# Kernel optimization log

Hardware: AMD Instinct MI355X
Metric: run time of the kernel (lower is better)

Reference implementation:

```python
import jax, jax.numpy as jnp
import numpy as np

ALPHA = 0.2  # LeakyReLU negative slope


def setup_inputs() -> dict:
    key = jax.random.key(0)
    k1, k2, k3, k4 = jax.random.split(key, 4)
    N, IN, OUT = 8192, 512, 256
    x = jax.random.normal(k1, (N, IN), dtype=jnp.float32)
    adj = jnp.zeros((N, N), dtype=jnp.float32)  # accepted but unused by the module
    W = jax.random.normal(k2, (OUT, IN), dtype=jnp.float32) * (1.0 / np.sqrt(IN))
    a1 = jax.random.normal(k3, (OUT,), dtype=jnp.float32) * (1.0 / np.sqrt(OUT))
    a2 = jax.random.normal(k4, (OUT,), dtype=jnp.float32) * (1.0 / np.sqrt(OUT))
    return {"x": x, "adj": adj, "W": W, "a1": a1, "a2": a2}


def reference(x, adj, W, a1, a2):
    # h = tran(x): [N, OUT]
    h = x @ W.T
    # additive GAT scores: e[i, j] = a2 . h_i + a1 . h_j  (from unsqueeze(0)+unsqueeze(1))
    s1 = h @ a1  # [N], att1(h)
    s2 = h @ a2  # [N], att2(h)
    e = s2[:, None] + s1[None, :]  # [N, N]
    e = jnp.where(e > 0, e, ALPHA * e)  # LeakyReLU
    attn = jax.nn.softmax(e, axis=1)  # softmax over dim=1; dropout is identity in eval
    return attn @ h  # [N, OUT]
```

## Files before the change

kernel.cpp:

```cpp
#include <hip/hip_runtime.h>

#define NROW 8192
#define DIN  512
#define DOUT 256
#define NCHUNK 256
#define CLEN 32

constexpr size_t OFF_H      = 0;
constexpr size_t OFF_S1     = OFF_H + (size_t)NROW*DOUT*4;
constexpr size_t OFF_S2     = OFF_S1 + NROW*4;
constexpr size_t OFF_RANK   = OFF_S2 + NROW*4;
constexpr size_t OFF_MISC   = OFF_RANK + NROW*4;
constexpr size_t MEMSET_LEN = OFF_MISC + 256 - OFF_S1;
constexpr size_t OFF_S1S    = OFF_MISC + 256;
constexpr size_t OFF_PERM   = OFF_S1S + NROW*4;
constexpr size_t OFF_WHI    = OFF_PERM + NROW*4;
constexpr size_t OFF_WLO    = OFF_WHI + NROW*4;
constexpr size_t OFF_PRELOS = OFF_WLO + NROW*4;
constexpr size_t OFF_SUFHIS = OFF_PRELOS + 33024;
constexpr size_t OFF_CSLO   = OFF_SUFHIS + 33024;
constexpr size_t OFF_CSHI   = OFF_CSLO + 1024;
constexpr size_t OFF_TLO    = OFF_CSHI + 1024;
constexpr size_t OFF_THI    = OFF_TLO + (size_t)NCHUNK*DOUT*4;
constexpr size_t OFF_PRELO  = OFF_THI + (size_t)NCHUNK*DOUT*4;
constexpr size_t OFF_SUFHI  = OFF_PRELO + (size_t)(NROW+1)*DOUT*4;
constexpr size_t WS_NEED    = OFF_SUFHI + (size_t)(NROW+1)*DOUT*4;

__global__ __launch_bounds__(256) void gemm_h(const float* __restrict__ x,
                                              const float* __restrict__ W,
                                              const float* __restrict__ a1,
                                              const float* __restrict__ a2,
                                              float* __restrict__ h,
                                              float* __restrict__ s1,
                                              float* __restrict__ s2) {
  __shared__ float xs[64][68];
  __shared__ float ws[64][68];
  const int tid = threadIdx.x;
  const int rowBase = blockIdx.x * 64;
  const int colBase = blockIdx.y * 64;
  const int ty = tid >> 4, tx = tid & 15;
  float acc[4][4] = {};
  for (int k0 = 0; k0 < DIN; k0 += 64) {
#pragma unroll
    for (int i = 0; i < 4; ++i) {
      int s = i * 256 + tid;
      int r = s >> 4;
      int kk = (s & 15) << 2;
      float4 v = *(const float4*)(x + (size_t)(rowBase + r) * DIN + k0 + kk);
      xs[kk + 0][r] = v.x; xs[kk + 1][r] = v.y; xs[kk + 2][r] = v.z; xs[kk + 3][r] = v.w;
      float4 u = *(const float4*)(W + (size_t)(colBase + r) * DIN + k0 + kk);
      ws[kk + 0][r] = u.x; ws[kk + 1][r] = u.y; ws[kk + 2][r] = u.z; ws[kk + 3][r] = u.w;
    }
    __syncthreads();
#pragma unroll
    for (int kk = 0; kk < 64; ++kk) {
      float4 av = *(const float4*)&xs[kk][ty << 2];
      float4 bv = *(const float4*)&ws[kk][tx << 2];
      float a[4] = {av.x, av.y, av.z, av.w};
      float b[4] = {bv.x, bv.y, bv.z, bv.w};
#pragma unroll
      for (int r = 0; r < 4; ++r)
#pragma unroll
        for (int c = 0; c < 4; ++c) acc[r][c] = fmaf(a[r], b[c], acc[r][c]);
    }
    __syncthreads();
  }
#pragma unroll
  for (int r = 0; r < 4; ++r) {
    float4 o = make_float4(acc[r][0], acc[r][1], acc[r][2], acc[r][3]);
    *(float4*)(h + (size_t)(rowBase + (ty << 2) + r) * DOUT + colBase + (tx << 2)) = o;
  }
  float4 A1 = *(const float4*)(a1 + colBase + (tx << 2));
  float4 A2 = *(const float4*)(a2 + colBase + (tx << 2));
#pragma unroll
  for (int r = 0; r < 4; ++r) {
    float p1 = acc[r][0] * A1.x + acc[r][1] * A1.y + acc[r][2] * A1.z + acc[r][3] * A1.w;
    float p2 = acc[r][0] * A2.x + acc[r][1] * A2.y + acc[r][2] * A2.z + acc[r][3] * A2.w;
#pragma unroll
    for (int m = 1; m < 16; m <<= 1) {
      p1 += __shfl_xor(p1, m);
      p2 += __shfl_xor(p2, m);
    }
    if (tx == 0) {
      int row = rowBase + (ty << 2) + r;
      atomicAdd(&s1[row], p1);
      atomicAdd(&s2[row], p2);
    }
  }
}

__global__ __launch_bounds__(256) void rank_count(const float* __restrict__ s1,
                                                  int* __restrict__ rank,
                                                  unsigned int* __restrict__ miscu) {
  __shared__ float sj[1024];
  __shared__ float wm[4];
  const int t = threadIdx.x;
  const int ib = blockIdx.x, jc = blockIdx.y;
  const int j0 = jc * 1024;
  *(float4*)&sj[t << 2] = *(const float4*)(s1 + j0 + (t << 2));
  const int i = ib * 256 + t;
  const float v = s1[i];
  __syncthreads();
  int cnt = 0;
#pragma unroll 4
  for (int q = 0; q < 256; ++q) {
    float4 sv = *(const float4*)&sj[q << 2];
    int jg = j0 + (q << 2);
    cnt += (int)(sv.x < v) + (int)((sv.x == v) & (jg + 0 < i));
    cnt += (int)(sv.y < v) + (int)((sv.y == v) & (jg + 1 < i));
    cnt += (int)(sv.z < v) + (int)((sv.z == v) & (jg + 2 < i));
    cnt += (int)(sv.w < v) + (int)((sv.w == v) & (jg + 3 < i));
  }
  atomicAdd(&rank[i], cnt);
  if (jc == 0) {
    float m = v;
#pragma unroll
    for (int off = 32; off > 0; off >>= 1) m = fmaxf(m, __shfl_down(m, off));
    if ((t & 63) == 0) wm[t >> 6] = m;
    __syncthreads();
    if (t == 0) {
      float mm = fmaxf(fmaxf(wm[0], wm[1]), fmaxf(wm[2], wm[3]));
      unsigned int b = __float_as_uint(mm);
      unsigned int enc = (b & 0x80000000u) ? ~b : (b | 0x80000000u);
      atomicMax(miscu, enc);
    }
  }
}

__global__ __launch_bounds__(256) void scatter_w(const float* __restrict__ s1,
                                                 const int* __restrict__ rank,
                                                 const unsigned int* __restrict__ miscu,
                                                 float* __restrict__ miscf,
                                                 float* __restrict__ s1s,
                                                 int* __restrict__ perm,
                                                 float* __restrict__ w_hi,
                                                 float* __restrict__ w_lo) {
  const int i = blockIdx.x * 256 + threadIdx.x;
  unsigned int e = miscu[0];
  unsigned int b = (e & 0x80000000u) ? (e & 0x7fffffffu) : ~e;
  const float M1 = __uint_as_float(b);
  const float v = s1[i];
  const int r = rank[i];
  s1s[r] = v;
  perm[r] = i;
  w_hi[r] = __expf(v - M1);
  w_lo[r] = __expf(0.2f * (v - M1));
  if (i == 0) miscf[0] = M1;
}

__global__ __launch_bounds__(256) void chunk_totals(const float* __restrict__ h,
                                                    const int* __restrict__ perm,
                                                    const float* __restrict__ w_hi,
                                                    const float* __restrict__ w_lo,
                                                    float* __restrict__ T_lo,
                                                    float* __restrict__ T_hi,
                                                    float* __restrict__ cs_lo,
                                                    float* __restrict__ cs_hi) {
  const int d = threadIdx.x, b = blockIdx.x;
  const int j0 = b * CLEN;
  float tlo = 0.f, thi = 0.f;
#pragma unroll
  for (int e = 0; e < CLEN; e += 4) {
    int4 p4 = *(const int4*)(perm + j0 + e);
    float4 wl4 = *(const float4*)(w_lo + j0 + e);
    float4 wh4 = *(const float4*)(w_hi + j0 + e);
    float h0 = h[(size_t)p4.x * DOUT + d];
    float h1 = h[(size_t)p4.y * DOUT + d];
    float h2 = h[(size_t)p4.z * DOUT + d];
    float h3 = h[(size_t)p4.w * DOUT + d];
    tlo += wl4.x * h0 + wl4.y * h1 + wl4.z * h2 + wl4.w * h3;
    thi += wh4.x * h0 + wh4.y * h1 + wh4.z * h2 + wh4.w * h3;
  }
  T_lo[b * DOUT + d] = tlo;
  T_hi[b * DOUT + d] = thi;
  if (d < 64) {
    float wl = (d < 32) ? w_lo[j0 + d] : 0.f;
    float wh = (d < 32) ? w_hi[j0 + d] : 0.f;
#pragma unroll
    for (int off = 32; off > 0; off >>= 1) {
      wl += __shfl_down(wl, off);
      wh += __shfl_down(wh, off);
    }
    if (d == 0) { cs_lo[b] = wl; cs_hi[b] = wh; }
  }
}

__global__ __launch_bounds__(256) void write_prefix(const float* __restrict__ h,
                                                    const int* __restrict__ perm,
                                                    const float* __restrict__ w_hi,
                                                    const float* __restrict__ w_lo,
                                                    const float* __restrict__ T_lo,
                                                    const float* __restrict__ T_hi,
                                                    const float* __restrict__ cs_lo,
                                                    const float* __restrict__ cs_hi,
                                                    float* __restrict__ PreLo,
                                                    float* __restrict__ SufHi,
                                                    float* __restrict__ prelo_s,
                                                    float* __restrict__ sufhi_s) {
  const int d = threadIdx.x, b = blockIdx.x;
  const int j0 = b * CLEN;
  if (d < 64) {
    float accp = 0.f, acct = 0.f;
    for (int p = d; p < NCHUNK; p += 64) {
      float cl = cs_lo[p], ch = cs_hi[p];
      accp += (p < b) ? cl : 0.f;
      acct += (p > b) ? ch : 0.f;
    }
#pragma unroll
    for (int off = 32; off > 0; off >>= 1) {
      accp += __shfl_down(accp, off);
      acct += __shfl_down(acct, off);
    }
    float pres  = __shfl(accp, 0);
    float tails = __shfl(acct, 0);
    float wl = (d < 32) ? w_lo[j0 + d] : 0.f;
    float wh = (d < 32) ? w_hi[j0 + d] : 0.f;
    float pl = wl, ph = wh;
#pragma unroll
    for (int off = 1; off < 32; off <<= 1) {
      float a = __shfl_up(pl, off);
      float c = __shfl_up(ph, off);
      if (d >= off) { pl += a; ph += c; }
    }
    float chunk_hi_tot = __shfl(ph, 31);
    if (d < 32) {
      prelo_s[j0 + d] = pres + (pl - wl);
      sufhi_s[j0 + d] = tails + (chunk_hi_tot - (ph - wh));
    }
    if (b == NCHUNK - 1 && d == 31) {
      prelo_s[NROW] = pres + pl;
      sufhi_s[NROW] = 0.f;
    }
  }
  float rl = 0.f, tail = 0.f;
#pragma unroll 8
  for (int p = 0; p < NCHUNK; ++p) {
    float vl = T_lo[p * DOUT + d];
    float vh = T_hi[p * DOUT + d];
    rl   += (p < b) ? vl : 0.f;
    tail += (p > b) ? vh : 0.f;
  }
  float hv[CLEN], wlv[CLEN], whv[CLEN];
  float ownHi = 0.f;
#pragma unroll
  for (int e = 0; e < CLEN; e += 4) {
    int4 p4 = *(const int4*)(perm + j0 + e);
    float4 wl4 = *(const float4*)(w_lo + j0 + e);
    float4 wh4 = *(const float4*)(w_hi + j0 + e);
    hv[e + 0] = h[(size_t)p4.x * DOUT + d];
    hv[e + 1] = h[(size_t)p4.y * DOUT + d];
    hv[e + 2] = h[(size_t)p4.z * DOUT + d];
    hv[e + 3] = h[(size_t)p4.w * DOUT + d];
    wlv[e + 0] = wl4.x; wlv[e + 1] = wl4.y; wlv[e + 2] = wl4.z; wlv[e + 3] = wl4.w;
    whv[e + 0] = wh4.x; whv[e + 1] = wh4.y; whv[e + 2] = wh4.z; whv[e + 3] = wh4.w;
    ownHi += wh4.x * hv[e] + wh4.y * hv[e + 1] + wh4.z * hv[e + 2] + wh4.w * hv[e + 3];
  }
  float shb = tail + ownHi;
  float preh = 0.f;
#pragma unroll
  for (int e = 0; e < CLEN; ++e) {
    size_t j = (size_t)(j0 + e);
    PreLo[j * DOUT + d] = rl;
    SufHi[j * DOUT + d] = shb - preh;
    rl   += wlv[e] * hv[e];
    preh += whv[e] * hv[e];
  }
  if (b == NCHUNK - 1) {
    PreLo[(size_t)NROW * DOUT + d] = rl;
    SufHi[(size_t)NROW * DOUT + d] = 0.f;
  }
}

__global__ __launch_bounds__(256) void finalize(const float* __restrict__ s2,
                                                const float* __restrict__ s1s,
                                                const float* __restrict__ miscf,
                                                const float* __restrict__ PreLo,
                                                const float* __restrict__ SufHi,
                                                const float* __restrict__ prelo_s,
                                                const float* __restrict__ sufhi_s,
                                                float* __restrict__ out) {
  const int wave = threadIdx.x >> 6, lane = threadIdx.x & 63;
  const int i = blockIdx.x * 4 + wave;
  const float c = s2[i];
  const float M1 = miscf[0];
  const float tval = -c;
  int lo = 0, hi = NROW;
  while (lo < hi) {
    int mid = (lo + hi) >> 1;
    if (s1s[mid] <= tval) lo = mid + 1; else hi = mid;
  }
  const int k = lo;
  const float u = c + M1;
  const float m = fmaxf(u, 0.2f * u);
  const float fh = __expf(u - m);
  const float fl = __expf(0.2f * u - m);
  const float den = fh * sufhi_s[k] + fl * prelo_s[k];
  const float inv = 1.f / den;
  float4 A = *(const float4*)(SufHi + (size_t)k * DOUT + (lane << 2));
  float4 B = *(const float4*)(PreLo + (size_t)k * DOUT + (lane << 2));
  float4 o;
  o.x = (fh * A.x + fl * B.x) * inv;
  o.y = (fh * A.y + fl * B.y) * inv;
  o.z = (fh * A.z + fl * B.z) * inv;
  o.w = (fh * A.w + fl * B.w) * inv;
  *(float4*)(out + (size_t)i * DOUT + (lane << 2)) = o;
}

extern "C" void kernel_launch(void* const* d_in, const int* in_sizes, int n_in,
                              void* d_out, int out_size, void* d_ws, size_t ws_size,
                              hipStream_t stream) {
  const float* x  = (const float*)d_in[0];
  const float* W  = (const float*)d_in[2];
  const float* a1 = (const float*)d_in[3];
  const float* a2 = (const float*)d_in[4];
  float* out = (float*)d_out;

  char* ws = (char*)d_ws;
  if (ws_size < WS_NEED) ws = (char*)d_in[1];

  float*        h       = (float*)(ws + OFF_H);
  float*        s1      = (float*)(ws + OFF_S1);
  float*        s2      = (float*)(ws + OFF_S2);
  int*          rank    = (int*)  (ws + OFF_RANK);
  unsigned int* miscu   = (unsigned int*)(ws + OFF_MISC);
  float*        miscf   = (float*)(ws + OFF_MISC) + 1;
  float*        s1s     = (float*)(ws + OFF_S1S);
  int*          perm    = (int*)  (ws + OFF_PERM);
  float*        w_hi    = (float*)(ws + OFF_WHI);
  float*        w_lo    = (float*)(ws + OFF_WLO);
  float*        prelo_s = (float*)(ws + OFF_PRELOS);
  float*        sufhi_s = (float*)(ws + OFF_SUFHIS);
  float*        cs_lo   = (float*)(ws + OFF_CSLO);
  float*        cs_hi   = (float*)(ws + OFF_CSHI);
  float*        T_lo    = (float*)(ws + OFF_TLO);
  float*        T_hi    = (float*)(ws + OFF_THI);
  float*        PreLo   = (float*)(ws + OFF_PRELO);
  float*        SufHi   = (float*)(ws + OFF_SUFHI);

  hipMemsetAsync(s1, 0, MEMSET_LEN, stream);

  gemm_h<<<dim3(NROW / 64, DOUT / 64), 256, 0, stream>>>(x, W, a1, a2, h, s1, s2);
  rank_count<<<dim3(NROW / 256, 8), 256, 0, stream>>>(s1, rank, miscu);
  scatter_w<<<NROW / 256, 256, 0, stream>>>(s1, rank, miscu, miscf, s1s, perm, w_hi, w_lo);
  chunk_totals<<<NCHUNK, 256, 0, stream>>>(h, perm, w_hi, w_lo, T_lo, T_hi, cs_lo, cs_hi);
  write_prefix<<<NCHUNK, 256, 0, stream>>>(h, perm, w_hi, w_lo, T_lo, T_hi, cs_lo, cs_hi,
                                           PreLo, SufHi, prelo_s, sufhi_s);
  finalize<<<NROW / 4, 256, 0, stream>>>(s2, s1s, miscf, PreLo, SufHi, prelo_s, sufhi_s, out);
}
```

Measured before the change: 405.7 us.

## Replace FP32 GEMM with split-bf16 three-pass MFMA and separate score kernel

Rewrites the x·Wᵀ GEMM to use bf16 MFMA 16x16x32 instructions. It emulates FP32 accuracy with a three-pass hi/lo split (hi·hi, lo·hi, hi·lo), converting operands to bf16 in registers while staging them to shared memory. The attention-score dot products s1/s2 are moved out of the GEMM epilogue into a separate per-row kernel, which removes the atomics. This costs an extra kernel launch and an extra read of h, and the split-bf16 scheme drops the lo·lo term, so precision is slightly reduced.

```diff
diff --git a/kernel.cpp b/kernel.cpp
--- a/kernel.cpp
+++ b/kernel.cpp
@@ -26,67 +26,110 @@
 constexpr size_t OFF_SUFHI  = OFF_PRELO + (size_t)(NROW+1)*DOUT*4;
 constexpr size_t WS_NEED    = OFF_SUFHI + (size_t)(NROW+1)*DOUT*4;
 
-__global__ __launch_bounds__(256) void gemm_h(const float* __restrict__ x,
-                                              const float* __restrict__ W,
-                                              const float* __restrict__ a1,
-                                              const float* __restrict__ a2,
-                                              float* __restrict__ h,
-                                              float* __restrict__ s1,
-                                              float* __restrict__ s2) {
-  __shared__ float xs[64][68];
-  __shared__ float ws[64][68];
+typedef float f32x4 __attribute__((ext_vector_type(4)));
+typedef short s16x8 __attribute__((ext_vector_type(8)));
+
+__device__ __forceinline__ unsigned short bf16_rne(float f) {
+  unsigned int u = __float_as_uint(f);
+  return (unsigned short)((u + 0x7fffu + ((u >> 16) & 1u)) >> 16);
+}
+__device__ __forceinline__ unsigned short bf16_part(float f, bool lo) {
+  unsigned short hi = bf16_rne(f);
+  if (!lo) return hi;
+  float r = f - __uint_as_float(((unsigned int)hi) << 16);
+  return bf16_rne(r);
+}
+__device__ __forceinline__ s16x8 cvt8(const float4 u, const float4 v, bool lo) {
+  s16x8 r;
+  r[0] = (short)bf16_part(u.x, lo); r[1] = (short)bf16_part(u.y, lo);
+  r[2] = (short)bf16_part(u.z, lo); r[3] = (short)bf16_part(u.w, lo);
+  r[4] = (short)bf16_part(v.x, lo); r[5] = (short)bf16_part(v.y, lo);
+  r[6] = (short)bf16_part(v.z, lo); r[7] = (short)bf16_part(v.w, lo);
+  return r;
+}
+
+__global__ __launch_bounds__(256) void gemm_h_mfma(const float* __restrict__ x,
+                                                   const float* __restrict__ W,
+                                                   float* __restrict__ h) {
+  __shared__ unsigned short As[64][40];
+  __shared__ unsigned short Bs[64][40];
   const int tid = threadIdx.x;
   const int rowBase = blockIdx.x * 64;
   const int colBase = blockIdx.y * 64;
-  const int ty = tid >> 4, tx = tid & 15;
-  float acc[4][4] = {};
-  for (int k0 = 0; k0 < DIN; k0 += 64) {
-#pragma unroll
-    for (int i = 0; i < 4; ++i) {
-      int s = i * 256 + tid;
-      int r = s >> 4;
-      int kk = (s & 15) << 2;
-      float4 v = *(const float4*)(x + (size_t)(rowBase + r) * DIN + k0 + kk);
-      xs[kk + 0][r] = v.x; xs[kk + 1][r] = v.y; xs[kk + 2][r] = v.z; xs[kk + 3][r] = v.w;
-      float4 u = *(const float4*)(W + (size_t)(colBase + r) * DIN + k0 + kk);
-      ws[kk + 0][r] = u.x; ws[kk + 1][r] = u.y; ws[kk + 2][r] = u.z; ws[kk + 3][r] = u.w;
-    }
-    __syncthreads();
-#pragma unroll
-    for (int kk = 0; kk < 64; ++kk) {
-      float4 av = *(const float4*)&xs[kk][ty << 2];
-      float4 bv = *(const float4*)&ws[kk][tx << 2];
-      float a[4] = {av.x, av.y, av.z, av.w};
-      float b[4] = {bv.x, bv.y, bv.z, bv.w};
-#pragma unroll
-      for (int r = 0; r < 4; ++r)
-#pragma unroll
-        for (int c = 0; c < 4; ++c) acc[r][c] = fmaf(a[r], b[c], acc[r][c]);
-    }
-    __syncthreads();
-  }
-#pragma unroll
-  for (int r = 0; r < 4; ++r) {
-    float4 o = make_float4(acc[r][0], acc[r][1], acc[r][2], acc[r][3]);
-    *(float4*)(h + (size_t)(rowBase + (ty << 2) + r) * DOUT + colBase + (tx << 2)) = o;
-  }
-  float4 A1 = *(const float4*)(a1 + colBase + (tx << 2));
-  float4 A2 = *(const float4*)(a2 + colBase + (tx << 2));
-#pragma unroll
-  for (int r = 0; r < 4; ++r) {
-    float p1 = acc[r][0] * A1.x + acc[r][1] * A1.y + acc[r][2] * A1.z + acc[r][3] * A1.w;
-    float p2 = acc[r][0] * A2.x + acc[r][1] * A2.y + acc[r][2] * A2.z + acc[r][3] * A2.w;
-#pragma unroll
-    for (int m = 1; m < 16; m <<= 1) {
-      p1 += __shfl_xor(p1, m);
-      p2 += __shfl_xor(p2, m);
-    }
-    if (tx == 0) {
-      int row = rowBase + (ty << 2) + r;
-      atomicAdd(&s1[row], p1);
-      atomicAdd(&s2[row], p2);
-    }
-  }
+  const int wid = tid >> 6, lane = tid & 63;
+  const int wRow = wid >> 1, wCol = wid & 1;
+  const int lhi = lane >> 4, llo = lane & 15;
+
+  f32x4 acc[2][2];
+#pragma unroll
+  for (int m = 0; m < 2; ++m)
+#pragma unroll
+    for (int n = 0; n < 2; ++n) acc[m][n] = (f32x4)(0.f);
+
+  const int sr = tid >> 2;
+  const int sq = tid & 3;
+  const float* xsrc = x + (size_t)(rowBase + sr) * DIN + sq * 8;
+  const float* wsrc = W + (size_t)(colBase + sr) * DIN + sq * 8;
+
+  for (int pass = 0; pass < 3; ++pass) {
+    const bool aLo = (pass == 1);
+    const bool bLo = (pass == 2);
+    for (int k0 = 0; k0 < DIN; k0 += 32) {
+      float4 a0 = *(const float4*)(xsrc + k0);
+      float4 a1v = *(const float4*)(xsrc + k0 + 4);
+      float4 b0 = *(const float4*)(wsrc + k0);
+      float4 b1 = *(const float4*)(wsrc + k0 + 4);
+      s16x8 av = cvt8(a0, a1v, aLo);
+      s16x8 bv = cvt8(b0, b1, bLo);
+      __syncthreads();
+      *(s16x8*)&As[sr][sq * 8] = av;
+      *(s16x8*)&Bs[sr][sq * 8] = bv;
+      __syncthreads();
+      s16x8 af[2], bf[2];
+#pragma unroll
+      for (int m = 0; m < 2; ++m)
+        af[m] = *(const s16x8*)&As[wRow * 32 + m * 16 + llo][lhi * 8];
+#pragma unroll
+      for (int n = 0; n < 2; ++n)
+        bf[n] = *(const s16x8*)&Bs[wCol * 32 + n * 16 + llo][lhi * 8];
+#pragma unroll
+      for (int m = 0; m < 2; ++m)
+#pragma unroll
+        for (int n = 0; n < 2; ++n)
+          acc[m][n] = __builtin_amdgcn_mfma_f32_16x16x32_bf16(af[m], bf[n], acc[m][n], 0, 0, 0);
+    }
+  }
+#pragma unroll
+  for (int m = 0; m < 2; ++m)
+#pragma unroll
+    for (int n = 0; n < 2; ++n) {
+      const int col = colBase + wCol * 32 + n * 16 + llo;
+#pragma unroll
+      for (int j = 0; j < 4; ++j) {
+        const int row = rowBase + wRow * 32 + m * 16 + lhi * 4 + j;
+        h[(size_t)row * DOUT + col] = acc[m][n][j];
+      }
+    }
+}
+
+__global__ __launch_bounds__(256) void s1s2_rows(const float* __restrict__ h,
+                                                 const float* __restrict__ a1,
+                                                 const float* __restrict__ a2,
+                                                 float* __restrict__ s1,
+                                                 float* __restrict__ s2) {
+  const int wid = threadIdx.x >> 6, lane = threadIdx.x & 63;
+  const int row = blockIdx.x * 4 + wid;
+  float4 hv = *(const float4*)(h + (size_t)row * DOUT + (lane << 2));
+  float4 A1 = *(const float4*)(a1 + (lane << 2));
+  float4 A2 = *(const float4*)(a2 + (lane << 2));
+  float p1 = hv.x * A1.x + hv.y * A1.y + hv.z * A1.z + hv.w * A1.w;
+  float p2 = hv.x * A2.x + hv.y * A2.y + hv.z * A2.z + hv.w * A2.w;
+#pragma unroll
+  for (int off = 32; off > 0; off >>= 1) {
+    p1 += __shfl_xor(p1, off);
+    p2 += __shfl_xor(p2, off);
+  }
+  if (lane == 0) { s1[row] = p1; s2[row] = p2; }
 }
 
 __global__ __launch_bounds__(256) void rank_count(const float* __restrict__ s1,
@@ -339,7 +382,8 @@
 
   hipMemsetAsync(s1, 0, MEMSET_LEN, stream);
 
-  gemm_h<<<dim3(NROW / 64, DOUT / 64), 256, 0, stream>>>(x, W, a1, a2, h, s1, s2);
+  gemm_h_mfma<<<dim3(NROW / 64, DOUT / 64), 256, 0, stream>>>(x, W, h);
+  s1s2_rows<<<NROW / 4, 256, 0, stream>>>(h, a1, a2, s1, s2);
   rank_count<<<dim3(NROW / 256, 8), 256, 0, stream>>>(s1, rank, miscu);
   scatter_w<<<NROW / 256, 256, 0, stream>>>(s1, rank, miscu, miscf, s1s, perm, w_hi, w_lo);
   chunk_totals<<<NCHUNK, 256, 0, stream>>>(h, perm, w_hi, w_lo, T_lo, T_hi, cs_lo, cs_hi);
```

Result: slower. 419.3 us (+3.4%).
